# Performance work log

Measured on AMD Instinct MI355X. Metric: run time of the kernel, lower is better.

The kernel has to match this reference:

```python
import jax, jax.numpy as jnp
import numpy as np

N_NODES = 50000
N_EDGES = 800000
IN_CH, HID_CH, OUT_CH = 128, 256, 256
N_LAYERS = 3


def setup_inputs() -> dict:
    key = jax.random.key(0)
    ks = jax.random.split(key, 9)
    x = jax.random.normal(ks[0], (N_NODES, IN_CH), dtype=jnp.float32)
    edge_index = jax.random.randint(ks[1], (2, N_EDGES), 0, N_NODES, dtype=jnp.int32)
    # Linear params, Kaiming-ish scale
    W1 = jax.random.normal(ks[2], (IN_CH, HID_CH), dtype=jnp.float32) / np.float32(np.sqrt(IN_CH))
    b1 = jnp.zeros((HID_CH,), jnp.float32)
    W2 = jax.random.normal(ks[3], (HID_CH, HID_CH), dtype=jnp.float32) / np.float32(np.sqrt(HID_CH))
    b2 = jnp.zeros((HID_CH,), jnp.float32)
    W3 = jax.random.normal(ks[4], (HID_CH, OUT_CH), dtype=jnp.float32) / np.float32(np.sqrt(HID_CH))
    b3 = jnp.zeros((OUT_CH,), jnp.float32)
    # learnable eps per GINConv (train_eps=True); small nonzero values for a nontrivial test
    eps = jax.random.normal(ks[5], (N_LAYERS,), dtype=jnp.float32) * 0.01
    return {"x": x, "edge_index": edge_index, "W1": W1, "b1": b1,
            "W2": W2, "b2": b2, "W3": W3, "b3": b3, "eps": eps}


def _gin_conv(x, src, dst, eps, W, b):
    # sum aggregation over incoming edges: agg[i] = sum_{(j->i)} x[j]
    agg = jax.ops.segment_sum(x[src], dst, num_segments=N_NODES)
    h = (1.0 + eps) * x + agg
    return h @ W + b


def reference(x, edge_index, W1, b1, W2, b2, W3, b3, eps):
    src, dst = edge_index[0], edge_index[1]
    # layers 0..L-2: conv -> relu -> dropout (identity in eval mode)
    h = jax.nn.relu(_gin_conv(x, src, dst, eps[0], W1, b1))
    h = jax.nn.relu(_gin_conv(h, src, dst, eps[1], W2, b2))
    # final layer: no relu
    out = _gin_conv(h, src, dst, eps[2], W3, b3)
    return out
```

## Files before the change

kernel.cpp:

```cpp
#include <hip/hip_runtime.h>


typedef __attribute__((ext_vector_type(8))) short short8;
typedef __attribute__((ext_vector_type(4))) float f32x4;

#define NBUK   256
#define BNODES 196

__device__ inline unsigned short f2bf(float f) {
    union { float f; unsigned u; } v; v.f = f;
    unsigned r = v.u + 0x7fffu + ((v.u >> 16) & 1u);
    return (unsigned short)(r >> 16);
}
__device__ inline float bflo(unsigned u) { return __uint_as_float(u << 16); }
__device__ inline float bfhi(unsigned u) { return __uint_as_float(u & 0xffff0000u); }

__device__ __forceinline__ void gload_lds16(const unsigned short* g, unsigned short* l) {
    __builtin_amdgcn_global_load_lds(
        (const __attribute__((address_space(1))) unsigned int*)g,
        (__attribute__((address_space(3))) unsigned int*)l,
        16, 0, 0);
}

#define ACC8(v) { acc[0]+=bflo(v.x); acc[1]+=bfhi(v.x); acc[2]+=bflo(v.y); acc[3]+=bfhi(v.y); \
                  acc[4]+=bflo(v.z); acc[5]+=bfhi(v.z); acc[6]+=bflo(v.w); acc[7]+=bfhi(v.w); }

__global__ __launch_bounds__(256) void prep_kernel(
    const float* __restrict__ x, const int* __restrict__ dst,
    const float* __restrict__ W1, const float* __restrict__ W2,
    const float* __restrict__ W3,
    unsigned short* __restrict__ xb, int* __restrict__ cnt,
    unsigned short* __restrict__ Ws1, unsigned short* __restrict__ Ws2,
    unsigned short* __restrict__ Ws3, int M, int nE)
{
    const int i  = blockIdx.x * 256 + threadIdx.x;
    const int nx = M * 16;
    if (i < nx) {
        const float4* xf = reinterpret_cast<const float4*>(x);
        float4 a = xf[2*i], b = xf[2*i + 1];
        uint4 o;
        o.x = (unsigned)f2bf(a.x) | ((unsigned)f2bf(a.y) << 16);
        o.y = (unsigned)f2bf(a.z) | ((unsigned)f2bf(a.w) << 16);
        o.z = (unsigned)f2bf(b.x) | ((unsigned)f2bf(b.y) << 16);
        o.w = (unsigned)f2bf(b.z) | ((unsigned)f2bf(b.w) << 16);
        const int node  = i >> 4;
        const int chunk = i & 15;
        const int cs    = chunk >> 2;
        const size_t idx = ((size_t)cs * M + node) * 32 + (chunk & 3) * 8;
        *reinterpret_cast<uint4*>(xb + idx) = o;
    } else if (i < nx + nE) {
        atomicAdd(&cnt[dst[i - nx]], 1);
    } else {
        int j = i - nx - nE;
        const float* W; unsigned short* D;
        if (j < 32768)       { W = W1; D = Ws1; }
        else if (j < 98304)  { W = W2; D = Ws2; j -= 32768; }
        else if (j < 163840) { W = W3; D = Ws3; j -= 98304; }
        else return;
        const int k = j >> 8, n = j & 255;
        D[((size_t)(k >> 3) * 256 + n) * 8 + (k & 7)] = f2bf(W[(size_t)k * 256 + n]);
    }
}


__global__ __launch_bounds__(1024) void scan1_kernel(
    const int* __restrict__ cnt, int* __restrict__ excl,
    int* __restrict__ bsum, int n)
{
    __shared__ int sh[1024];
    const int tid = threadIdx.x;
    const int i = blockIdx.x * 1024 + tid;
    int v = (i < n) ? cnt[i] : 0;
    sh[tid] = v;
    __syncthreads();
    #pragma unroll
    for (int off = 1; off < 1024; off <<= 1) {
        int t = (tid >= off) ? sh[tid - off] : 0;
        __syncthreads();
        sh[tid] += t;
        __syncthreads();
    }
    if (i < n) excl[i] = sh[tid] - v;
    if (tid == 1023) bsum[blockIdx.x] = sh[1023];
}

__global__ __launch_bounds__(1024) void scan3_kernel(
    const int* __restrict__ excl, const int* __restrict__ bsum,
    int* __restrict__ row_start, int* __restrict__ gcur,
    int n, int nE, int nbl)
{
    __shared__ int sb[64];
    const int tid = threadIdx.x;
    if (tid < 64) sb[tid] = (tid < nbl) ? bsum[tid] : 0;
    __syncthreads();
    #pragma unroll
    for (int off = 1; off < 64; off <<= 1) {
        int v = 0;
        if (tid < 64 && tid >= off) v = sb[tid - off];
        __syncthreads();
        if (tid < 64) sb[tid] += v;
        __syncthreads();
    }
    const int boff = sb[blockIdx.x] - bsum[blockIdx.x];
    const int i = blockIdx.x * 1024 + tid;
    if (i < n) {
        int v = excl[i] + boff;
        row_start[i] = v;
        if ((i % BNODES) == 0) gcur[i / BNODES] = v;
    }
    if (i == 0) row_start[n] = nE;
}


__global__ __launch_bounds__(256) void binA_kernel(
    const int* __restrict__ src, const int* __restrict__ dst,
    int* __restrict__ gcur, unsigned* __restrict__ pair_buf, int nE)
{
    __shared__ int lhist[NBUK];
    __shared__ int lbase[NBUK];
    const int t = threadIdx.x;
    lhist[t] = 0;
    __syncthreads();

    const int e0 = blockIdx.x * 4096;
    int d[16], s[16], r[16];
    #pragma unroll
    for (int i = 0; i < 16; ++i) {
        const int e = e0 + i * 256 + t;
        if (e < nE) {
            d[i] = dst[e];
            s[i] = src[e];
            r[i] = atomicAdd(&lhist[d[i] / BNODES], 1);
        }
    }
    __syncthreads();
    lbase[t] = lhist[t] ? atomicAdd(&gcur[t], lhist[t]) : 0;
    __syncthreads();
    #pragma unroll
    for (int i = 0; i < 16; ++i) {
        const int e = e0 + i * 256 + t;
        if (e < nE)
            pair_buf[lbase[d[i] / BNODES] + r[i]] =
                ((unsigned)d[i] << 16) | (unsigned)s[i];
    }
}

__global__ __launch_bounds__(256) void binB_kernel(
    const unsigned* __restrict__ pair_buf, const int* __restrict__ row_start,
    unsigned short* __restrict__ adj, int M)
{
    __shared__ int lcur[BNODES];
    const int b   = blockIdx.x;
    const int nb0 = b * BNODES;
    const int nb1 = min(nb0 + BNODES, M);
    const int nn  = nb1 - nb0;
    const int t   = threadIdx.x;
    if (nn <= 0) return;
    for (int i = t; i < nn; i += 256) lcur[i] = row_start[nb0 + i];
    __syncthreads();
    const int p0 = row_start[nb0];
    const int p1 = row_start[nb1];
    for (int p = p0 + t; p < p1; p += 256) {
        const unsigned pr = pair_buf[p];
        const int dn = (int)(pr >> 16);
        const int pos = atomicAdd(&lcur[dn - nb0], 1);
        adj[pos] = (unsigned short)(pr & 0xFFFFu);
    }
}


template <int CIN, int NSLICE>
__global__ __launch_bounds__(256) void agg_sliced(
    const unsigned short* __restrict__ Xcs,
    const int* __restrict__ row_start, const unsigned short* __restrict__ adj,
    const float* __restrict__ eps_arr, int layer,
    unsigned short* __restrict__ H, int M)
{
    constexpr int SHIFT = (NSLICE == 8) ? 3 : 2;

    const int cs   = blockIdx.x & (NSLICE - 1);
    const int grp  = blockIdx.x >> SHIFT;
    const int node = grp * 64 + (threadIdx.x >> 2);
    const int c8   = threadIdx.x & 3;
    if (node >= M) return;

    const uint4* __restrict__ X4 =
        reinterpret_cast<const uint4*>(Xcs) + (size_t)cs * M * 4;

    float acc[8] = {};
    const int s0 = row_start[node];
    const int s1 = row_start[node + 1];
    const int deg = s1 - s0;

    int j = s0;
    if (deg >= 4) {
        const int jend = s0 + (deg & ~3);
        int a0 = adj[j], a1 = adj[j+1], a2 = adj[j+2], a3 = adj[j+3];
        uint4 p0 = X4[(size_t)a0 * 4 + c8];
        uint4 p1 = X4[(size_t)a1 * 4 + c8];
        uint4 p2 = X4[(size_t)a2 * 4 + c8];
        uint4 p3 = X4[(size_t)a3 * 4 + c8];
        for (j += 4; j < jend; j += 4) {
            const int b0 = adj[j], b1 = adj[j+1], b2 = adj[j+2], b3 = adj[j+3];
            const uint4 n0 = X4[(size_t)b0 * 4 + c8];
            const uint4 n1 = X4[(size_t)b1 * 4 + c8];
            const uint4 n2 = X4[(size_t)b2 * 4 + c8];
            const uint4 n3 = X4[(size_t)b3 * 4 + c8];
            ACC8(p0); ACC8(p1); ACC8(p2); ACC8(p3);
            p0 = n0; p1 = n1; p2 = n2; p3 = n3;
        }
        ACC8(p0); ACC8(p1); ACC8(p2); ACC8(p3);
    }
    for (; j < s1; ++j) {
        const uint4 v = X4[(size_t)adj[j] * 4 + c8];
        ACC8(v);
    }

    const uint4 xv = X4[(size_t)node * 4 + c8];
    const float epsv = 1.0f + eps_arr[layer];
    float o[8];
    o[0] = epsv * bflo(xv.x) + acc[0]; o[1] = epsv * bfhi(xv.x) + acc[1];
    o[2] = epsv * bflo(xv.y) + acc[2]; o[3] = epsv * bfhi(xv.y) + acc[3];
    o[4] = epsv * bflo(xv.z) + acc[4]; o[5] = epsv * bfhi(xv.z) + acc[5];
    o[6] = epsv * bflo(xv.w) + acc[6]; o[7] = epsv * bfhi(xv.w) + acc[7];

    uint4 ov;
    ov.x = (unsigned)f2bf(o[0]) | ((unsigned)f2bf(o[1]) << 16);
    ov.y = (unsigned)f2bf(o[2]) | ((unsigned)f2bf(o[3]) << 16);
    ov.z = (unsigned)f2bf(o[4]) | ((unsigned)f2bf(o[5]) << 16);
    ov.w = (unsigned)f2bf(o[6]) | ((unsigned)f2bf(o[7]) << 16);
    *reinterpret_cast<uint4*>(H + (size_t)node * CIN + cs * 32 + c8 * 8) = ov;
}

template <int CIN, int RELU, int OUTMODE>
__global__ __launch_bounds__(256) void gemm_tiled(
    const unsigned short* __restrict__ H, const unsigned short* __restrict__ Wsub,
    const float* __restrict__ bias, void* __restrict__ out, int M)
{
    constexpr int S = CIN / 32;

    __shared__ __align__(16) unsigned short As[2][4][64][8];

    const int t    = threadIdx.x;
    const int bm   = blockIdx.x * 64;
    const int w    = t >> 6, lane = t & 63;
    const int lr   = lane & 15, ko = lane >> 4;

    const int srow = t & 63;
    const int skb  = t >> 6;
    const unsigned short* aG = H + (size_t)(bm + srow) * CIN + skb * 8;

    f32x4 acc[4][4];
    #pragma unroll
    for (int fn = 0; fn < 4; ++fn) {
        const float bb = bias[w*64 + fn*16 + lr];
        #pragma unroll
        for (int fm = 0; fm < 4; ++fm) {
            acc[fm][fn][0] = bb; acc[fm][fn][1] = bb;
            acc[fm][fn][2] = bb; acc[fm][fn][3] = bb;
        }
    }

    gload_lds16(aG, &As[0][skb][srow][0]);

    int cur = 0;
    for (int s = 0; s < S; ++s) {
        __syncthreads();
        if (s + 1 < S)
            gload_lds16(aG + (s+1)*32, &As[cur ^ 1][skb][srow][0]);

        short8 af[4], bf8[4];
        #pragma unroll
        for (int fm = 0; fm < 4; ++fm)
            af[fm] = *reinterpret_cast<const short8*>(&As[cur][ko][fm*16 + lr][0]);
        #pragma unroll
        for (int fn = 0; fn < 4; ++fn)
            bf8[fn] = *reinterpret_cast<const short8*>(
                Wsub + ((size_t)(s*4 + ko) * 256 + w*64 + fn*16 + lr) * 8);
        #pragma unroll
        for (int fm = 0; fm < 4; ++fm)
            #pragma unroll
            for (int fn = 0; fn < 4; ++fn)
                acc[fm][fn] = __builtin_amdgcn_mfma_f32_16x16x32_bf16(
                    af[fm], bf8[fn], acc[fm][fn], 0, 0, 0);

        cur ^= 1;
    }

    #pragma unroll
    for (int fm = 0; fm < 4; ++fm) {
        #pragma unroll
        for (int fn = 0; fn < 4; ++fn) {
            const int col = w*64 + fn*16 + lr;
            #pragma unroll
            for (int r = 0; r < 4; ++r) {
                const int row = bm + fm*16 + ko*4 + r;
                if (row < M) {
                    float v = acc[fm][fn][r];
                    if (RELU) v = fmaxf(v, 0.f);
                    if (OUTMODE == 1) {
                        ((unsigned short*)out)[(size_t)(col >> 5) * M * 32
                                               + (size_t)row * 32 + (col & 31)] = f2bf(v);
                    } else {
                        ((float*)out)[(size_t)row * 256 + col] = v;
                    }
                }
            }
        }
    }
}


extern "C" void kernel_launch(void* const* d_in, const int* in_sizes, int n_in,
                              void* d_out, int out_size, void* d_ws, size_t ws_size,
                              hipStream_t stream)
{
    const float* x   = (const float*)d_in[0];
    const int*   ei  = (const int*)  d_in[1];
    const float* W1  = (const float*)d_in[2];
    const float* b1  = (const float*)d_in[3];
    const float* W2  = (const float*)d_in[4];
    const float* b2  = (const float*)d_in[5];
    const float* W3  = (const float*)d_in[6];
    const float* b3  = (const float*)d_in[7];
    const float* eps = (const float*)d_in[8];

    const int M  = in_sizes[0] / 128;
    const int nE = in_sizes[1] / 2;
    const int Mp = ((M + 63) / 64) * 64;
    const int* srcI = ei;
    const int* dstI = ei + nE;

    char* p = (char*)d_ws;
    unsigned short* xb_cs = (unsigned short*)p; p += (size_t)M  * 128 * 2;
    unsigned short* Arow  = (unsigned short*)p; p += (size_t)Mp * 256 * 2;
    unsigned short* s_cs  = (unsigned short*)p; p += (size_t)M  * 256 * 2;
    unsigned short* Ws1   = (unsigned short*)p; p += (size_t)128 * 256 * 2;
    unsigned short* Ws2   = (unsigned short*)p; p += (size_t)256 * 256 * 2;
    unsigned short* Ws3   = (unsigned short*)p; p += (size_t)256 * 256 * 2;
    int* cnt       = (int*)p; p += (size_t)M * 4;
    int* excl      = (int*)p; p += (size_t)M * 4;
    int* bsum      = (int*)p; p += 64 * 4;
    int* gcur      = (int*)p; p += NBUK * 4;
    int* row_start = (int*)p; p += (size_t)(M + 2) * 4;
    unsigned* pair_buf = (unsigned*)p; p += (size_t)nE * 4;
    unsigned short* adj = (unsigned short*)p; p += (size_t)nE * 2;

    const int nbl = (M + 1023) / 1024;

    hipMemsetAsync(cnt, 0, (size_t)M * sizeof(int), stream);
    {
        const int total = M * 16 + nE + 163840;
        prep_kernel<<<(total + 255) / 256, 256, 0, stream>>>(
            x, dstI, W1, W2, W3, xb_cs, cnt, Ws1, Ws2, Ws3, M, nE);
    }
    scan1_kernel<<<nbl, 1024, 0, stream>>>(cnt, excl, bsum, M);
    scan3_kernel<<<nbl, 1024, 0, stream>>>(excl, bsum, row_start, gcur, M, nE, nbl);
    binA_kernel<<<(nE + 4095) / 4096, 256, 0, stream>>>(srcI, dstI, gcur, pair_buf, nE);
    binB_kernel<<<NBUK, 256, 0, stream>>>(pair_buf, row_start, adj, M);

    const int ablk1 = 4 * ((M + 63) / 64);
    const int ablk2 = 8 * ((M + 63) / 64);
    const int gblk  = Mp / 64;

    agg_sliced<128, 4><<<ablk1, 256, 0, stream>>>(xb_cs, row_start, adj, eps, 0, Arow, M);
    gemm_tiled<128, 1, 1><<<gblk, 256, 0, stream>>>(Arow, Ws1, b1, s_cs, M);

    agg_sliced<256, 8><<<ablk2, 256, 0, stream>>>(s_cs, row_start, adj, eps, 1, Arow, M);
    gemm_tiled<256, 1, 1><<<gblk, 256, 0, stream>>>(Arow, Ws2, b2, s_cs, M);

    agg_sliced<256, 8><<<ablk2, 256, 0, stream>>>(s_cs, row_start, adj, eps, 2, Arow, M);
    gemm_tiled<256, 0, 0><<<gblk, 256, 0, stream>>>(Arow, Ws3, b3, d_out, M);
}
```

Before: 249.7 us.

## Process aggregation nodes in degree-sorted order to balance per-wavefront work

Builds a degree histogram and counting sort of nodes by in-degree (capped at 255) during the CSR scans. The aggregation kernels then read node ids through this permutation, so each wavefront handles nodes of similar degree and loop trip counts diverge less. The cost is an extra tiny kernel, global atomics in the scan kernels, and scattered writes and reads of the output rows, which may hurt locality.

```diff
diff --git a/kernel.cpp b/kernel.cpp
--- a/kernel.cpp
+++ b/kernel.cpp
@@ -65,12 +65,13 @@
 
 __global__ __launch_bounds__(1024) void scan1_kernel(
     const int* __restrict__ cnt, int* __restrict__ excl,
-    int* __restrict__ bsum, int n)
+    int* __restrict__ bsum, int* __restrict__ dhist, int n)
 {
     __shared__ int sh[1024];
     const int tid = threadIdx.x;
     const int i = blockIdx.x * 1024 + tid;
     int v = (i < n) ? cnt[i] : 0;
+    if (i < n) atomicAdd(&dhist[v > 255 ? 255 : v], 1);
     sh[tid] = v;
     __syncthreads();
     #pragma unroll
@@ -84,8 +85,28 @@
     if (tid == 1023) bsum[blockIdx.x] = sh[1023];
 }
 
+__global__ __launch_bounds__(256) void dscan_kernel(
+    const int* __restrict__ dhist, int* __restrict__ dcur)
+{
+    __shared__ int sh[256];
+    const int t = threadIdx.x;
+    int v = dhist[t];
+    sh[t] = v;
+    __syncthreads();
+    #pragma unroll
+    for (int off = 1; off < 256; off <<= 1) {
+        int u = (t >= off) ? sh[t - off] : 0;
+        __syncthreads();
+        sh[t] += u;
+        __syncthreads();
+    }
+    dcur[t] = sh[t] - v;
+}
+
 __global__ __launch_bounds__(1024) void scan3_kernel(
     const int* __restrict__ excl, const int* __restrict__ bsum,
+    const int* __restrict__ cnt, int* __restrict__ dcur,
+    int* __restrict__ perm,
     int* __restrict__ row_start, int* __restrict__ gcur,
     int n, int nE, int nbl)
 {
@@ -107,6 +128,9 @@
         int v = excl[i] + boff;
         row_start[i] = v;
         if ((i % BNODES) == 0) gcur[i / BNODES] = v;
+        int d = cnt[i]; if (d > 255) d = 255;
+        const int pos = atomicAdd(&dcur[d], 1);
+        perm[pos] = i;
     }
     if (i == 0) row_start[n] = nE;
 }
@@ -173,6 +197,7 @@
 __global__ __launch_bounds__(256) void agg_sliced(
     const unsigned short* __restrict__ Xcs,
     const int* __restrict__ row_start, const unsigned short* __restrict__ adj,
+    const int* __restrict__ perm,
     const float* __restrict__ eps_arr, int layer,
     unsigned short* __restrict__ H, int M)
 {
@@ -180,9 +205,10 @@
 
     const int cs   = blockIdx.x & (NSLICE - 1);
     const int grp  = blockIdx.x >> SHIFT;
-    const int node = grp * 64 + (threadIdx.x >> 2);
+    const int nidx = grp * 64 + (threadIdx.x >> 2);
     const int c8   = threadIdx.x & 3;
-    if (node >= M) return;
+    if (nidx >= M) return;
+    const int node = perm[nidx];
 
     const uint4* __restrict__ X4 =
         reinterpret_cast<const uint4*>(Xcs) + (size_t)cs * M * 4;
@@ -339,6 +365,9 @@
     unsigned short* Ws2   = (unsigned short*)p; p += (size_t)256 * 256 * 2;
     unsigned short* Ws3   = (unsigned short*)p; p += (size_t)256 * 256 * 2;
     int* cnt       = (int*)p; p += (size_t)M * 4;
+    int* dhist     = (int*)p; p += 256 * 4;
+    int* dcur      = (int*)p; p += 256 * 4;
+    int* perm      = (int*)p; p += (size_t)M * 4;
     int* excl      = (int*)p; p += (size_t)M * 4;
     int* bsum      = (int*)p; p += 64 * 4;
     int* gcur      = (int*)p; p += NBUK * 4;
@@ -348,14 +377,16 @@
 
     const int nbl = (M + 1023) / 1024;
 
-    hipMemsetAsync(cnt, 0, (size_t)M * sizeof(int), stream);
+    hipMemsetAsync(cnt, 0, ((size_t)M + 256) * sizeof(int), stream);
     {
         const int total = M * 16 + nE + 163840;
         prep_kernel<<<(total + 255) / 256, 256, 0, stream>>>(
             x, dstI, W1, W2, W3, xb_cs, cnt, Ws1, Ws2, Ws3, M, nE);
     }
-    scan1_kernel<<<nbl, 1024, 0, stream>>>(cnt, excl, bsum, M);
-    scan3_kernel<<<nbl, 1024, 0, stream>>>(excl, bsum, row_start, gcur, M, nE, nbl);
+    scan1_kernel<<<nbl, 1024, 0, stream>>>(cnt, excl, bsum, dhist, M);
+    dscan_kernel<<<1, 256, 0, stream>>>(dhist, dcur);
+    scan3_kernel<<<nbl, 1024, 0, stream>>>(excl, bsum, cnt, dcur, perm,
+                                           row_start, gcur, M, nE, nbl);
     binA_kernel<<<(nE + 4095) / 4096, 256, 0, stream>>>(srcI, dstI, gcur, pair_buf, nE);
     binB_kernel<<<NBUK, 256, 0, stream>>>(pair_buf, row_start, adj, M);
 
@@ -363,12 +394,12 @@
     const int ablk2 = 8 * ((M + 63) / 64);
     const int gblk  = Mp / 64;
 
-    agg_sliced<128, 4><<<ablk1, 256, 0, stream>>>(xb_cs, row_start, adj, eps, 0, Arow, M);
+    agg_sliced<128, 4><<<ablk1, 256, 0, stream>>>(xb_cs, row_start, adj, perm, eps, 0, Arow, M);
     gemm_tiled<128, 1, 1><<<gblk, 256, 0, stream>>>(Arow, Ws1, b1, s_cs, M);
 
-    agg_sliced<256, 8><<<ablk2, 256, 0, stream>>>(s_cs, row_start, adj, eps, 1, Arow, M);
+    agg_sliced<256, 8><<<ablk2, 256, 0, stream>>>(s_cs, row_start, adj, perm, eps, 1, Arow, M);
     gemm_tiled<256, 1, 1><<<gblk, 256, 0, stream>>>(Arow, Ws2, b2, s_cs, M);
 
-    agg_sliced<256, 8><<<ablk2, 256, 0, stream>>>(s_cs, row_start, adj, eps, 2, Arow, M);
+    agg_sliced<256, 8><<<ablk2, 256, 0, stream>>>(s_cs, row_start, adj, perm, eps, 2, Arow, M);
     gemm_tiled<256, 0, 0><<<gblk, 256, 0, stream>>>(Arow, Ws3, b3, d_out, M);
 }
```

After: 490.3 us. 1.96x slower.
